# Kernel tuning notes

Hardware: AMD Instinct MI355X
Metric: run time of the kernel (lower is better)

The kernel has to match this reference:

```python
import jax, jax.numpy as jnp
import numpy as np

D_MODEL = 512
D_FFN = 1024
B, N = 8, 2048


def setup_inputs() -> dict:
    key = jax.random.key(0)
    k1, k2, k3, k4, k5, k6 = jax.random.split(key, 6)
    x = jax.random.normal(k1, (B, N, D_MODEL), dtype=jnp.float32)
    interaction_mask = jax.random.randint(k2, (B, N, N), 0, 2).astype(jnp.float32)
    s1 = 1.0 / np.sqrt(D_MODEL)
    s2 = 1.0 / np.sqrt(D_FFN)
    W1 = jax.random.uniform(k3, (D_MODEL, D_FFN), jnp.float32, -s1, s1)
    b1 = jax.random.uniform(k4, (D_FFN,), jnp.float32, -s1, s1)
    W2 = jax.random.uniform(k5, (D_FFN, 3 * D_MODEL), jnp.float32, -s2, s2)
    b2 = jax.random.uniform(k6, (3 * D_MODEL,), jnp.float32, -s2, s2)
    return {"x": x, "interaction_mask": interaction_mask,
            "W1": W1, "b1": b1, "W2": W2, "b2": b2}


def reference(x, interaction_mask, W1, b1, W2, b2):
    # 2-layer FFN: Linear -> ReLU -> Linear (identity)
    h = jax.nn.relu(x @ W1 + b1)           # [B, N, d_ffn]
    kqv = h @ W2 + b2                        # [B, N, 3*d_model]
    k, q, v = jnp.split(kqv, 3, axis=-1)     # each [B, N, d_model]
    scale = D_MODEL ** -0.5
    # softmax-free scaled dot-product
    attn = jnp.einsum("bqd,bkd->bqk", q, k) * scale  # [B, N, N]
    attn = attn * interaction_mask
    return jnp.einsum("bqk,bkd->bqd", attn, v)        # [B, N, d_model]
```

## Files before the change

### kernel.cpp

```cpp
#include <hip/hip_runtime.h>
#include <hip/hip_bf16.h>

typedef __attribute__((ext_vector_type(8))) short bf16x8;
typedef __attribute__((ext_vector_type(4))) float f32x4;

#define NB 8
#define NN 2048
#define DM 512
#define DF 1024

__device__ __forceinline__ ushort f2b(float f) {
  union { __hip_bfloat16 h; ushort u; } c;
  c.h = __float2bfloat16(f);
  return c.u;
}
__device__ __forceinline__ float b2f(ushort u) {
  union { ushort u; __hip_bfloat16 h; } c;
  c.u = u;
  return __bfloat162float(c.h);
}

typedef __attribute__((address_space(1))) const void gvoid_t;
typedef __attribute__((address_space(3))) void svoid_t;
__device__ __forceinline__ void gload16(const void* g, void* s) {
  __builtin_amdgcn_global_load_lds((gvoid_t*)g, (svoid_t*)s, 16, 0, 0);
}

__device__ __forceinline__ void gemm_core_128(
    const ushort* __restrict__ A, const ushort* __restrict__ B,
    int K, int brow, int bcol, f32x4 (&acc)[4][4], ushort* smem)
{
  const int tid = threadIdx.x;
  const int w = tid >> 6, l = tid & 63;
  const int sr = (w << 3) + (l >> 3);
  const int sc = (((l & 7) ^ (l >> 3)) << 3);
  const int fr = l & 15;
  const int arow = ((w >> 1) << 6) + fr;
  const int brw  = ((w & 1) << 6) + fr;
  char* base = (char*)smem;
  char* A0 = base;          char* B0 = base + 16384;
  char* A1 = base + 32768;  char* B1 = base + 49152;

#pragma unroll
  for (int m = 0; m < 4; m++)
#pragma unroll
    for (int n = 0; n < 4; n++)
      acc[m][n] = (f32x4){0.f, 0.f, 0.f, 0.f};

  const ushort* Ap = A + (long)(brow + sr) * K + sc;
  const ushort* Bp = B + (long)(bcol + sr) * K + sc;
  const int nkt = K >> 6;

  auto stage = [&](char* Ad, char* Bd, int kt) {
#pragma unroll
    for (int i = 0; i < 4; i++) {
      gload16(Ap + (long)i * 32 * K + kt * 64, Ad + i * 4096 + (w << 10));
      gload16(Bp + (long)i * 32 * K + kt * 64, Bd + i * 4096 + (w << 10));
    }
  };
  auto compute = [&](const char* As_, const char* Bs_) {
#pragma unroll
    for (int kk = 0; kk < 2; kk++) {
      const int cx = ((((kk << 2) + (l >> 4)) ^ (l & 7)) << 4);
      bf16x8 a[4], b[4];
#pragma unroll
      for (int m = 0; m < 4; m++)
        a[m] = *(const bf16x8*)(As_ + (arow + m * 16) * 128 + cx);
#pragma unroll
      for (int n = 0; n < 4; n++)
        b[n] = *(const bf16x8*)(Bs_ + (brw + n * 16) * 128 + cx);
#pragma unroll
      for (int m = 0; m < 4; m++)
#pragma unroll
        for (int n = 0; n < 4; n++)
          acc[m][n] = __builtin_amdgcn_mfma_f32_16x16x32_bf16(a[m], b[n], acc[m][n], 0, 0, 0);
    }
  };

  stage(A0, B0, 0);
  __syncthreads();
  for (int kt = 0; kt < nkt; kt += 2) {
    stage(A1, B1, kt + 1);
    compute(A0, B0);
    __syncthreads();
    if (kt + 2 < nkt) stage(A0, B0, kt + 2);
    compute(A1, B1);
    __syncthreads();
  }
}

__device__ __forceinline__ void acc_to_lds_bf16(f32x4 (&acc)[4][4], ushort* smem) {
  const int tid = threadIdx.x, w = tid >> 6, l = tid & 63;
  const int r0l = ((w >> 1) << 6) + ((l >> 4) << 2);
  const int c0l = ((w & 1) << 6) + (l & 15);
#pragma unroll
  for (int n = 0; n < 4; n++)
#pragma unroll
    for (int m = 0; m < 4; m++)
#pragma unroll
      for (int j = 0; j < 4; j++)
        smem[(r0l + m * 16 + j) * 128 + (c0l + n * 16)] = f2b(acc[m][n][j]);
}


__global__ __launch_bounds__(256) void k_cvt(const float* __restrict__ in,
                                             ushort* __restrict__ out) {
  const long i = ((long)blockIdx.x * 256 + threadIdx.x) << 2;
  const float4 v = *(const float4*)(in + i);
  ushort4 o;
  o.x = f2b(v.x); o.y = f2b(v.y); o.z = f2b(v.z); o.w = f2b(v.w);
  *(ushort4*)(out + i) = o;
}

__device__ __forceinline__ float ld2f(const float* p, long i) { return p[i]; }
__device__ __forceinline__ float ld2f(const __hip_bfloat16* p, long i) { return __bfloat162float(p[i]); }

template <typename TIN>
__global__ __launch_bounds__(256) void k_tr(const TIN* __restrict__ in, ushort* __restrict__ out,
                                            int R, int C, long inB, long outB) {
  __shared__ float t[32][33];
  const long b = blockIdx.z;
  const TIN* ip = in + b * inB;
  ushort* op = out + b * outB;
  const int c0 = blockIdx.x << 5, r0 = blockIdx.y << 5;
  const int tx = threadIdx.x & 31, ty = threadIdx.x >> 5;
#pragma unroll
  for (int j = 0; j < 32; j += 8)
    t[ty + j][tx] = ld2f(ip, (long)(r0 + ty + j) * C + (c0 + tx));
  __syncthreads();
#pragma unroll
  for (int j = 0; j < 32; j += 8)
    op[(long)(c0 + ty + j) * R + (r0 + tx)] = f2b(t[tx][ty + j]);
}

__global__ __launch_bounds__(256) void k_gemm1(const ushort* __restrict__ xb,
                                               const ushort* __restrict__ w1t,
                                               const float* __restrict__ b1,
                                               ushort* __restrict__ hb) {
  __shared__ ushort smem[128 * 256];
  f32x4 acc[4][4];
  const int brow = blockIdx.x << 7, bcol = blockIdx.y << 7;
  gemm_core_128(xb, w1t, DM, brow, bcol, acc, smem);
  const int tid = threadIdx.x, w = tid >> 6, l = tid & 63;
  const int c0l = ((w & 1) << 6) + (l & 15);
#pragma unroll
  for (int n = 0; n < 4; n++) {
    const float bias = b1[bcol + c0l + n * 16];
#pragma unroll
    for (int m = 0; m < 4; m++)
#pragma unroll
      for (int j = 0; j < 4; j++) {
        float v = acc[m][n][j] + bias;
        acc[m][n][j] = v > 0.f ? v : 0.f;
      }
  }
  acc_to_lds_bf16(acc, smem);
  __syncthreads();
  const int rb = tid >> 4, cb = tid & 15;
#pragma unroll
  for (int i = 0; i < 8; i++) {
    const int row = i * 16 + rb;
    bf16x8 s = *(const bf16x8*)(smem + row * 128 + cb * 8);
    *(bf16x8*)(hb + (long)(brow + row) * DF + bcol + cb * 8) = s;
  }
}

__global__ __launch_bounds__(256) void k_gemm2(const ushort* __restrict__ hb,
                                               const ushort* __restrict__ w2t,
                                               const float* __restrict__ b2,
                                               ushort* __restrict__ kb,
                                               ushort* __restrict__ qb,
                                               ushort* __restrict__ vb) {
  __shared__ ushort smem[128 * 256];
  f32x4 acc[4][4];
  const int brow = blockIdx.x << 7, bcol = blockIdx.y << 7;
  gemm_core_128(hb, w2t, DF, brow, bcol, acc, smem);
  const int seg = bcol >> 9;
  ushort* dst = (seg == 0) ? kb : ((seg == 1) ? qb : vb);
  const float sc = (seg == 1) ? 0.04419417382415922f : 1.0f;
  const int tid = threadIdx.x, w = tid >> 6, l = tid & 63;
  const int c0l = ((w & 1) << 6) + (l & 15);
#pragma unroll
  for (int n = 0; n < 4; n++) {
    const float bias = b2[bcol + c0l + n * 16];
#pragma unroll
    for (int m = 0; m < 4; m++)
#pragma unroll
      for (int j = 0; j < 4; j++)
        acc[m][n][j] = (acc[m][n][j] + bias) * sc;
  }
  acc_to_lds_bf16(acc, smem);
  __syncthreads();
  const int rb = tid >> 4, cb = tid & 15;
  const int clb = bcol - (seg << 9);
#pragma unroll
  for (int i = 0; i < 8; i++) {
    const int row = i * 16 + rb;
    bf16x8 s = *(const bf16x8*)(smem + row * 128 + cb * 8);
    *(bf16x8*)(dst + (long)(brow + row) * DM + clb + cb * 8) = s;
  }
}

__global__ __launch_bounds__(256) void k_qk(const ushort* __restrict__ qb,
                                            const ushort* __restrict__ kb,
                                            const float* __restrict__ mask,
                                            ushort* __restrict__ Sbuf) {
  __shared__ ushort smem[128 * 256];
  const int orig = blockIdx.x;
  const int swz = (orig & 7) * 256 + (orig >> 3);
  const int bx = swz & 15, by = (swz >> 4) & 15, batch = swz >> 8;
  const int brow = bx << 7, bcol = by << 7;
  const ushort* A = qb + (long)batch * NN * DM;
  const ushort* Bm = kb + (long)batch * NN * DM;
  const float* mk = mask + (long)batch * NN * NN;
  ushort* S = Sbuf + (long)batch * NN * NN;

  const int tid = threadIdx.x, rb = tid >> 4, cb = tid & 15;
  float4 mreg[8][2];
#pragma unroll
  for (int i = 0; i < 8; i++) {
    const long goff = (long)(brow + i * 16 + rb) * NN + bcol + cb * 8;
    mreg[i][0] = *(const float4*)(mk + goff);
    mreg[i][1] = *(const float4*)(mk + goff + 4);
  }

  f32x4 acc[4][4];
  gemm_core_128(A, Bm, DM, brow, bcol, acc, smem);
  acc_to_lds_bf16(acc, smem);
  __syncthreads();
#pragma unroll
  for (int i = 0; i < 8; i++) {
    const int row = i * 16 + rb;
    const long goff = (long)(brow + row) * NN + bcol + cb * 8;
    bf16x8 s = *(const bf16x8*)(smem + row * 128 + cb * 8);
    bf16x8 o;
    o[0] = (short)f2b(b2f((ushort)s[0]) * mreg[i][0].x);
    o[1] = (short)f2b(b2f((ushort)s[1]) * mreg[i][0].y);
    o[2] = (short)f2b(b2f((ushort)s[2]) * mreg[i][0].z);
    o[3] = (short)f2b(b2f((ushort)s[3]) * mreg[i][0].w);
    o[4] = (short)f2b(b2f((ushort)s[4]) * mreg[i][1].x);
    o[5] = (short)f2b(b2f((ushort)s[5]) * mreg[i][1].y);
    o[6] = (short)f2b(b2f((ushort)s[6]) * mreg[i][1].z);
    o[7] = (short)f2b(b2f((ushort)s[7]) * mreg[i][1].w);
    *(bf16x8*)(S + goff) = o;
  }
}

__global__ __launch_bounds__(256) void k_pv(const ushort* __restrict__ Sbuf,
                                            const ushort* __restrict__ vtb,
                                            float* __restrict__ out) {
  __shared__ ushort smem[128 * 256];
  const int batch = blockIdx.z;
  const ushort* A = Sbuf + (long)batch * NN * NN;
  const ushort* Bm = vtb + (long)batch * DM * NN;
  float* op = out + (long)batch * NN * DM;
  f32x4 acc[4][4];
  const int brow = blockIdx.x << 7, bcol = blockIdx.y << 7;
  gemm_core_128(A, Bm, NN, brow, bcol, acc, smem);
  const int tid = threadIdx.x, w = tid >> 6, l = tid & 63;
  const int r0 = brow + ((w >> 1) << 6) + ((l >> 4) << 2);
  const int c0 = bcol + ((w & 1) << 6) + (l & 15);
#pragma unroll
  for (int n = 0; n < 4; n++) {
    const int c = c0 + n * 16;
#pragma unroll
    for (int m = 0; m < 4; m++) {
      const int r = r0 + m * 16;
#pragma unroll
      for (int j = 0; j < 4; j++)
        op[(long)(r + j) * DM + c] = acc[m][n][j];
    }
  }
}

extern "C" void kernel_launch(void* const* d_in, const int* in_sizes, int n_in,
                              void* d_out, int out_size, void* d_ws, size_t ws_size,
                              hipStream_t stream) {
  const float* x    = (const float*)d_in[0];
  const float* mask = (const float*)d_in[1];
  const float* W1   = (const float*)d_in[2];
  const float* b1   = (const float*)d_in[3];
  const float* W2   = (const float*)d_in[4];
  const float* b2   = (const float*)d_in[5];
  float* out = (float*)d_out;

  char* ws = (char*)d_ws;
  size_t off = 0;
  auto alloc = [&](size_t n) { char* p = ws + off; off += (n + 255) & ~(size_t)255; return p; };
  ushort* xb  = (ushort*)alloc((size_t)NB * NN * DM * 2);
  ushort* hb  = (ushort*)alloc((size_t)NB * NN * DF * 2);
  ushort* w1t = (ushort*)alloc((size_t)DF * DM * 2);
  ushort* w2t = (ushort*)alloc((size_t)3 * DM * DF * 2);
  ushort* kb  = (ushort*)alloc((size_t)NB * NN * DM * 2);
  ushort* qb  = (ushort*)alloc((size_t)NB * NN * DM * 2);
  ushort* vb  = (ushort*)alloc((size_t)NB * NN * DM * 2);
  ushort* vtb = (ushort*)alloc((size_t)NB * NN * DM * 2);
  ushort* Sbuf = (ushort*)alloc((size_t)NB * NN * NN * 2);

  k_cvt<<<dim3(8192), dim3(256), 0, stream>>>(x, xb);
  k_tr<float><<<dim3(DF / 32, DM / 32, 1), dim3(256), 0, stream>>>(W1, w1t, DM, DF, 0, 0);
  k_tr<float><<<dim3(3 * DM / 32, DF / 32, 1), dim3(256), 0, stream>>>(W2, w2t, DF, 3 * DM, 0, 0);
  k_gemm1<<<dim3(NB * NN / 128, DF / 128), dim3(256), 0, stream>>>(xb, w1t, b1, hb);
  k_gemm2<<<dim3(NB * NN / 128, 3 * DM / 128), dim3(256), 0, stream>>>(hb, w2t, b2, kb, qb, vb);
  k_tr<__hip_bfloat16><<<dim3(DM / 32, NN / 32, NB), dim3(256), 0, stream>>>(
      (const __hip_bfloat16*)vb, vtb, NN, DM, (long)NN * DM, (long)DM * NN);
  k_qk<<<dim3(2048), dim3(256), 0, stream>>>(qb, kb, mask, Sbuf);
  k_pv<<<dim3(NN / 128, DM / 128, NB), dim3(256), 0, stream>>>(Sbuf, vtb, out);
}
```

Before: 221.1 us.

## Rewrite QK^T masked kernel with 256x256 tiles and double-buffered LDS pipeline

```diff
diff --git a/kernel.cpp b/kernel.cpp
--- a/kernel.cpp
+++ b/kernel.cpp
@@ -201,48 +201,121 @@
   }
 }
 
-__global__ __launch_bounds__(256) void k_qk(const ushort* __restrict__ qb,
-                                            const ushort* __restrict__ kb,
-                                            const float* __restrict__ mask,
-                                            ushort* __restrict__ Sbuf) {
-  __shared__ ushort smem[128 * 256];
-  const int orig = blockIdx.x;
-  const int swz = (orig & 7) * 256 + (orig >> 3);
-  const int bx = swz & 15, by = (swz >> 4) & 15, batch = swz >> 8;
-  const int brow = bx << 7, bcol = by << 7;
+__global__ __launch_bounds__(512, 2) void k_qk256(const ushort* __restrict__ qb,
+                                                  const ushort* __restrict__ kb,
+                                                  const float* __restrict__ mask,
+                                                  ushort* __restrict__ Sbuf) {
+  __shared__ ushort smem[65536];
+  const int bid = blockIdx.x;
+  const int batch = bid & 7;
+  const int tile = bid >> 3;
+  const int brow = (tile & 7) << 8, bcol = (tile >> 3) << 8;
   const ushort* A = qb + (long)batch * NN * DM;
-  const ushort* Bm = kb + (long)batch * NN * DM;
+  const ushort* B = kb + (long)batch * NN * DM;
+  const int K = DM;
+
+  const int tid = threadIdx.x;
+  const int w = tid >> 6, l = tid & 63;
+  const int wr = w >> 2, wc = w & 3;
+  const int fr = l & 15;
+  char* bufbase = (char*)smem;
+
+  f32x4 acc[8][4];
+#pragma unroll
+  for (int m = 0; m < 8; m++)
+#pragma unroll
+    for (int n = 0; n < 4; n++)
+      acc[m][n] = (f32x4){0.f, 0.f, 0.f, 0.f};
+
+  const int srow = (w << 3) + (l >> 3);
+  const int sc = (((l & 7) ^ (l >> 3)) << 3);
+
+  auto stage_half = [&](int b, int kt, int mat, int h) {
+    const ushort* P = mat ? B : A;
+    const int rbase = (mat ? bcol : brow) + (h << 7);
+    char* dst = bufbase + (b << 16) + (mat << 15) + (h << 14) + (w << 10);
+#pragma unroll
+    for (int i = 0; i < 2; i++)
+      gload16(P + (long)(rbase + (i << 6) + srow) * K + (kt << 6) + sc,
+              dst + (i << 13));
+  };
+
+  stage_half(0, 0, 0, 0); stage_half(0, 0, 0, 1);
+  stage_half(0, 0, 1, 0); stage_half(0, 0, 1, 1);
+  __syncthreads();
+
+  const int nkt = K >> 6;
+  for (int kt = 0; kt < nkt; ++kt) {
+    const int b = kt & 1;
+    const char* cA = bufbase + (b << 16);
+    const char* cB = cA + 32768;
+    const bool pre = (kt + 1 < nkt);
+#pragma unroll
+    for (int kk = 0; kk < 2; ++kk) {
+      const int cx = ((((kk << 2) + (l >> 4)) ^ (l & 7)) << 4);
+      bf16x8 bfrag[4];
+#pragma unroll
+      for (int n = 0; n < 4; n++)
+        bfrag[n] = *(const bf16x8*)(cB + ((wc << 6) + (n << 4) + fr) * 128 + cx);
+#pragma unroll
+      for (int mh = 0; mh < 2; ++mh) {
+        if (kk == 0 && pre) {
+          stage_half(b ^ 1, kt + 1, mh, 0);
+          stage_half(b ^ 1, kt + 1, mh, 1);
+        }
+        bf16x8 afrag[4];
+#pragma unroll
+        for (int mi = 0; mi < 4; mi++)
+          afrag[mi] = *(const bf16x8*)(cA + ((wr << 7) + (mh << 6) + (mi << 4) + fr) * 128 + cx);
+        __builtin_amdgcn_s_setprio(1);
+#pragma unroll
+        for (int mi = 0; mi < 4; mi++)
+#pragma unroll
+          for (int n = 0; n < 4; n++)
+            acc[mh * 4 + mi][n] =
+                __builtin_amdgcn_mfma_f32_16x16x32_bf16(afrag[mi], bfrag[n], acc[mh * 4 + mi][n], 0, 0, 0);
+        __builtin_amdgcn_s_setprio(0);
+      }
+    }
+    __syncthreads();
+  }
+
+#pragma unroll
+  for (int m = 0; m < 8; m++)
+#pragma unroll
+    for (int n = 0; n < 4; n++)
+#pragma unroll
+      for (int j = 0; j < 4; j++) {
+        const int row = (wr << 7) + (m << 4) + ((l >> 4) << 2) + j;
+        const int col = (wc << 6) + (n << 4) + fr;
+        smem[row * 256 + (col ^ ((row & 7) << 3))] = f2b(acc[m][n][j]);
+      }
+  __syncthreads();
+
   const float* mk = mask + (long)batch * NN * NN;
   ushort* S = Sbuf + (long)batch * NN * NN;
-
-  const int tid = threadIdx.x, rb = tid >> 4, cb = tid & 15;
-  float4 mreg[8][2];
-#pragma unroll
-  for (int i = 0; i < 8; i++) {
-    const long goff = (long)(brow + i * 16 + rb) * NN + bcol + cb * 8;
-    mreg[i][0] = *(const float4*)(mk + goff);
-    mreg[i][1] = *(const float4*)(mk + goff + 4);
-  }
-
-  f32x4 acc[4][4];
-  gemm_core_128(A, Bm, DM, brow, bcol, acc, smem);
-  acc_to_lds_bf16(acc, smem);
-  __syncthreads();
-#pragma unroll
-  for (int i = 0; i < 8; i++) {
-    const int row = i * 16 + rb;
-    const long goff = (long)(brow + row) * NN + bcol + cb * 8;
-    bf16x8 s = *(const bf16x8*)(smem + row * 128 + cb * 8);
-    bf16x8 o;
-    o[0] = (short)f2b(b2f((ushort)s[0]) * mreg[i][0].x);
-    o[1] = (short)f2b(b2f((ushort)s[1]) * mreg[i][0].y);
-    o[2] = (short)f2b(b2f((ushort)s[2]) * mreg[i][0].z);
-    o[3] = (short)f2b(b2f((ushort)s[3]) * mreg[i][0].w);
-    o[4] = (short)f2b(b2f((ushort)s[4]) * mreg[i][1].x);
-    o[5] = (short)f2b(b2f((ushort)s[5]) * mreg[i][1].y);
-    o[6] = (short)f2b(b2f((ushort)s[6]) * mreg[i][1].z);
-    o[7] = (short)f2b(b2f((ushort)s[7]) * mreg[i][1].w);
-    *(bf16x8*)(S + goff) = o;
+  const int rr = tid >> 4, cc = tid & 15;
+#pragma unroll
+  for (int i = 0; i < 8; ++i) {
+    const int row = (i << 5) + rr;
+    const long gr = (long)(brow + row) * NN + bcol;
+#pragma unroll
+    for (int hf = 0; hf < 2; ++hf) {
+      const int ch = (hf << 4) + cc;
+      bf16x8 s = *(const bf16x8*)(smem + row * 256 + ((ch ^ (row & 7)) << 3));
+      const float4 m0 = *(const float4*)(mk + gr + ch * 8);
+      const float4 m1 = *(const float4*)(mk + gr + ch * 8 + 4);
+      bf16x8 o;
+      o[0] = (short)f2b(b2f((ushort)s[0]) * m0.x);
+      o[1] = (short)f2b(b2f((ushort)s[1]) * m0.y);
+      o[2] = (short)f2b(b2f((ushort)s[2]) * m0.z);
+      o[3] = (short)f2b(b2f((ushort)s[3]) * m0.w);
+      o[4] = (short)f2b(b2f((ushort)s[4]) * m1.x);
+      o[5] = (short)f2b(b2f((ushort)s[5]) * m1.y);
+      o[6] = (short)f2b(b2f((ushort)s[6]) * m1.z);
+      o[7] = (short)f2b(b2f((ushort)s[7]) * m1.w);
+      *(bf16x8*)(S + gr + ch * 8) = o;
+    }
   }
 }
 
@@ -304,6 +377,6 @@
   k_gemm2<<<dim3(NB * NN / 128, 3 * DM / 128), dim3(256), 0, stream>>>(hb, w2t, b2, kb, qb, vb);
   k_tr<__hip_bfloat16><<<dim3(DM / 32, NN / 32, NB), dim3(256), 0, stream>>>(
       (const __hip_bfloat16*)vb, vtb, NN, DM, (long)NN * DM, (long)DM * NN);
-  k_qk<<<dim3(2048), dim3(256), 0, stream>>>(qb, kb, mask, Sbuf);
+  k_qk256<<<dim3(512), dim3(512), 0, stream>>>(qb, kb, mask, Sbuf);
   k_pv<<<dim3(NN / 128, DM / 128, NB), dim3(256), 0, stream>>>(Sbuf, vtb, out);
 }
```

Result: slower. 227.4 us (+2.8%).
